# Optimization experiments

Measured on AMD Instinct MI355X. Metric: run time of the kernel, lower is better.

## Reference

```python
import jax, jax.numpy as jnp
import numpy as np


def setup_inputs() -> dict:
    key = jax.random.key(0)
    k1, k2, k3, k4, k5 = jax.random.split(key, 5)
    N, L, V = 8, 2048, 512
    E = 2 * V
    tokens = jax.random.randint(k1, (N, L, E), 0, 2, dtype=jnp.int64)
    s = 1.0 / np.sqrt(E)
    Wa_w = jax.random.uniform(k2, (E, E), jnp.float32, -s, s)
    Wa_b = jax.random.uniform(k3, (E,), jnp.float32, -s, s)
    Wb_w = jax.random.uniform(k4, (V, E), jnp.float32, -s, s)
    Wb_b = jax.random.uniform(k5, (V,), jnp.float32, -s, s)
    return {"tokens": tokens, "Wa_w": Wa_w, "Wa_b": Wa_b, "Wb_w": Wb_w, "Wb_b": Wb_b}


def reference(tokens, Wa_w, Wa_b, Wb_w, Wb_b):
    # x: [N, L, E] float embedding of binary tokens
    x = tokens.astype(jnp.float32)
    # q = Wa(x): [N, L, E] (torch Linear: x @ W^T + b)
    q = jnp.einsum("nle,fe->nlf", x, Wa_w) + Wa_b
    # scores: [N, L, L]; softmax over last dim
    scores = jnp.einsum("nlf,nmf->nlm", q, x)
    wts = jax.nn.softmax(scores, axis=-1)
    # a = wts @ x: [N, L, E]
    a = jnp.einsum("nlm,nme->nle", wts, x)
    # y = Wb(a): [N, L, V]; logits from last position
    y = jnp.einsum("nle,ve->nlv", a, Wb_w) + Wb_b
    logits = y[:, -1]  # [N, V]
    return logits
```

## Files before the change

### kernel.cpp

```cpp
#include <hip/hip_runtime.h>

#define NB 8
#define LS 2048
#define ED 1024
#define VD 512
#define CM 32
#define CH (LS / CM)
typedef unsigned long long u64;

__device__ inline float wave_reduce_sum(float v) {
    #pragma unroll
    for (int off = 32; off > 0; off >>= 1)
        v += __shfl_down(v, off, 64);
    return v;
}

__global__ void k_qrow(const int* __restrict__ tokens, const float* __restrict__ Wa_w,
                       const float* __restrict__ Wa_b, float* __restrict__ q_row) {
    int wid  = blockIdx.x * (blockDim.x >> 6) + (threadIdx.x >> 6);
    int lane = threadIdx.x & 63;
    int n = wid >> 10;
    int f = wid & (ED - 1);
    const int*   xrow = tokens + ((size_t)n * LS + (LS - 1)) * ED;
    const float* wrow = Wa_w + (size_t)f * ED;
    float acc = 0.f;
    #pragma unroll
    for (int k = 0; k < ED; k += 256) {
        int idx = k + lane * 4;
        int4   t = *reinterpret_cast<const int4*>(xrow + idx);
        float4 w = *reinterpret_cast<const float4*>(wrow + idx);
        acc += (float)t.x * w.x + (float)t.y * w.y + (float)t.z * w.z + (float)t.w * w.w;
    }
    acc = wave_reduce_sum(acc);
    if (lane == 0) q_row[wid] = acc + Wa_b[f];
}

__global__ __launch_bounds__(512) void k_flash(const int* __restrict__ tokens,
                                               const float* __restrict__ q_row,
                                               float* __restrict__ pa,
                                               float* __restrict__ mu_g,
                                               float* __restrict__ z_g) {
    int n = blockIdx.x >> 6;
    int c = blockIdx.x & (CH - 1);
    int t = threadIdx.x;
    int wave = t >> 6, lane = t & 63;

    __shared__ u64   pk[CM][16];
    __shared__ float s_lds[CM];
    __shared__ float p_lds[CM];

    const float* q = q_row + n * ED;

    #pragma unroll
    for (int i = 0; i < 4; ++i) {
        int m = wave + 8 * i;
        const int* row = tokens + ((size_t)(n * LS + c * CM + m)) * ED;
        float acc = 0.f;
        #pragma unroll
        for (int k = 0; k < ED; k += 256) {
            int idx = k + lane * 4;
            int4   tv = *reinterpret_cast<const int4*>(row + idx);
            float4 qv = *reinterpret_cast<const float4*>(q + idx);
            u64 b0 = __ballot(tv.x != 0);
            u64 b1 = __ballot(tv.y != 0);
            u64 b2 = __ballot(tv.z != 0);
            u64 b3 = __ballot(tv.w != 0);
            if (lane == 0) {
                int wb = (k >> 8) * 4;
                pk[m][wb + 0] = b0; pk[m][wb + 1] = b1;
                pk[m][wb + 2] = b2; pk[m][wb + 3] = b3;
            }
            acc += (float)tv.x * qv.x + (float)tv.y * qv.y
                 + (float)tv.z * qv.z + (float)tv.w * qv.w;
        }
        acc = wave_reduce_sum(acc);
        if (lane == 0) s_lds[m] = acc;
    }
    __syncthreads();

    if (wave == 0) {
        float s = (lane < CM) ? s_lds[lane] : -3.0e38f;
        float mx = s;
        #pragma unroll
        for (int off = 16; off > 0; off >>= 1) mx = fmaxf(mx, __shfl_xor(mx, off, 64));
        float p = (lane < CM) ? expf(s - mx) : 0.f;
        float z = p;
        #pragma unroll
        for (int off = 16; off > 0; off >>= 1) z += __shfl_xor(z, off, 64);
        if (lane < CM) p_lds[lane] = p;
        if (lane == 0) { mu_g[blockIdx.x] = mx; z_g[blockIdx.x] = z; }
    }
    __syncthreads();

    int w0  = ((t >> 8) << 2) | (t & 3);
    int bit = (t >> 2) & 63;
    float a0 = 0.f, a1 = 0.f;
    #pragma unroll 8
    for (int m = 0; m < CM; ++m) {
        float p  = p_lds[m];
        u64   lo = pk[m][w0];
        u64   hi = pk[m][w0 + 8];
        a0 += ((lo >> bit) & 1ull) ? p : 0.f;
        a1 += ((hi >> bit) & 1ull) ? p : 0.f;
    }
    float* par = pa + (size_t)blockIdx.x * ED;
    par[t]       = a0;
    par[t + 512] = a1;
}

__global__ __launch_bounds__(1024) void k_out(const float* __restrict__ pa,
                                              const float* __restrict__ mu_g,
                                              const float* __restrict__ z_g,
                                              const float* __restrict__ Wb_w,
                                              const float* __restrict__ Wb_b,
                                              float* __restrict__ out) {
    int n  = blockIdx.x >> 4;
    int vt = blockIdx.x & 15;
    int t  = threadIdx.x;
    int wave = t >> 6, lane = t & 63;
    __shared__ float coef[CH];
    __shared__ float a_lds[ED];

    if (wave == 0) {
        float m_c = mu_g[n * CH + lane];
        float mx = m_c;
        #pragma unroll
        for (int off = 32; off > 0; off >>= 1) mx = fmaxf(mx, __shfl_xor(mx, off, 64));
        float cf = expf(m_c - mx);
        float zc = z_g[n * CH + lane] * cf;
        float Z = zc;
        #pragma unroll
        for (int off = 32; off > 0; off >>= 1) Z += __shfl_xor(Z, off, 64);
        coef[lane] = cf / Z;
    }
    __syncthreads();

    float acc = 0.f;
    #pragma unroll
    for (int ci = 0; ci < CH; ++ci)
        acc += coef[ci] * pa[((size_t)(n * CH + ci)) * ED + t];
    a_lds[t] = acc;
    __syncthreads();

    #pragma unroll
    for (int i = 0; i < 2; ++i) {
        int v = vt * 32 + wave * 2 + i;
        const float* wr = Wb_w + (size_t)v * ED;
        float d = 0.f;
        #pragma unroll
        for (int k = 0; k < ED; k += 256) {
            int idx = k + lane * 4;
            float4 wv = *reinterpret_cast<const float4*>(wr + idx);
            float4 av = *reinterpret_cast<const float4*>(&a_lds[idx]);
            d += av.x * wv.x + av.y * wv.y + av.z * wv.z + av.w * wv.w;
        }
        d = wave_reduce_sum(d);
        if (lane == 0) out[n * VD + v] = d + Wb_b[v];
    }
}

extern "C" void kernel_launch(void* const* d_in, const int* in_sizes, int n_in,
                              void* d_out, int out_size, void* d_ws, size_t ws_size,
                              hipStream_t stream) {
    const int*   tokens = (const int*)  d_in[0];
    const float* Wa_w   = (const float*)d_in[1];
    const float* Wa_b   = (const float*)d_in[2];
    const float* Wb_w   = (const float*)d_in[3];
    const float* Wb_b   = (const float*)d_in[4];
    float* out = (float*)d_out;

    float* ws    = (float*)d_ws;
    float* q_row = ws;
    float* pa    = q_row + NB * ED;
    float* mu_g  = pa + (size_t)NB * CH * ED;
    float* z_g   = mu_g + NB * CH;

    k_qrow<<<dim3((NB * ED) / 4), dim3(256), 0, stream>>>(tokens, Wa_w, Wa_b, q_row);
    k_flash<<<dim3(NB * CH), dim3(512), 0, stream>>>(tokens, q_row, pa, mu_g, z_g);
    k_out<<<dim3(NB * 16), dim3(1024), 0, stream>>>(pa, mu_g, z_g, Wb_w, Wb_b, out);
}
```

Baseline: 31.61 us.

## Batch qrow over all batches per weight row, stage q in LDS, nontemporal token loads

```diff
diff --git a/kernel.cpp b/kernel.cpp
--- a/kernel.cpp
+++ b/kernel.cpp
@@ -7,6 +7,7 @@
 #define CM 32
 #define CH (LS / CM)
 typedef unsigned long long u64;
+typedef __attribute__((ext_vector_type(4))) int i32x4;
 
 __device__ inline float wave_reduce_sum(float v) {
     #pragma unroll
@@ -15,24 +16,41 @@
     return v;
 }
 
-__global__ void k_qrow(const int* __restrict__ tokens, const float* __restrict__ Wa_w,
-                       const float* __restrict__ Wa_b, float* __restrict__ q_row) {
-    int wid  = blockIdx.x * (blockDim.x >> 6) + (threadIdx.x >> 6);
-    int lane = threadIdx.x & 63;
-    int n = wid >> 10;
-    int f = wid & (ED - 1);
-    const int*   xrow = tokens + ((size_t)n * LS + (LS - 1)) * ED;
+__global__ __launch_bounds__(256) void k_qrow(const int* __restrict__ tokens,
+                                              const float* __restrict__ Wa_w,
+                                              const float* __restrict__ Wa_b,
+                                              float* __restrict__ q_row) {
+    __shared__ int xs[NB][ED];
+    int t = threadIdx.x;
+    #pragma unroll
+    for (int i = 0; i < 8; ++i) {
+        int v4 = i * 256 + t;
+        int n  = v4 >> 8;
+        int e  = (v4 & 255) * 4;
+        *reinterpret_cast<int4*>(&xs[n][e]) =
+            *reinterpret_cast<const int4*>(&tokens[((size_t)n * LS + (LS - 1)) * ED + e]);
+    }
+    __syncthreads();
+    int wave = t >> 6, lane = t & 63;
+    int f = blockIdx.x * 4 + wave;
     const float* wrow = Wa_w + (size_t)f * ED;
-    float acc = 0.f;
+    float acc[NB] = {0.f, 0.f, 0.f, 0.f, 0.f, 0.f, 0.f, 0.f};
     #pragma unroll
     for (int k = 0; k < ED; k += 256) {
         int idx = k + lane * 4;
-        int4   t = *reinterpret_cast<const int4*>(xrow + idx);
         float4 w = *reinterpret_cast<const float4*>(wrow + idx);
-        acc += (float)t.x * w.x + (float)t.y * w.y + (float)t.z * w.z + (float)t.w * w.w;
-    }
-    acc = wave_reduce_sum(acc);
-    if (lane == 0) q_row[wid] = acc + Wa_b[f];
+        #pragma unroll
+        for (int n = 0; n < NB; ++n) {
+            int4 tv = *reinterpret_cast<const int4*>(&xs[n][idx]);
+            acc[n] += (float)tv.x * w.x + (float)tv.y * w.y
+                    + (float)tv.z * w.z + (float)tv.w * w.w;
+        }
+    }
+    #pragma unroll
+    for (int n = 0; n < NB; ++n) {
+        float s = wave_reduce_sum(acc[n]);
+        if (lane == 0) q_row[n * ED + f] = s + Wa_b[f];
+    }
 }
 
 __global__ __launch_bounds__(512) void k_flash(const int* __restrict__ tokens,
@@ -46,10 +64,13 @@
     int wave = t >> 6, lane = t & 63;
 
     __shared__ u64   pk[CM][16];
+    __shared__ float q_lds[ED];
     __shared__ float s_lds[CM];
     __shared__ float p_lds[CM];
 
-    const float* q = q_row + n * ED;
+    *reinterpret_cast<float2*>(&q_lds[t * 2]) =
+        *reinterpret_cast<const float2*>(&q_row[n * ED + t * 2]);
+    __syncthreads();
 
     #pragma unroll
     for (int i = 0; i < 4; ++i) {
@@ -59,8 +80,8 @@
         #pragma unroll
         for (int k = 0; k < ED; k += 256) {
             int idx = k + lane * 4;
-            int4   tv = *reinterpret_cast<const int4*>(row + idx);
-            float4 qv = *reinterpret_cast<const float4*>(q + idx);
+            i32x4  tv = __builtin_nontemporal_load(reinterpret_cast<const i32x4*>(row + idx));
+            float4 qv = *reinterpret_cast<const float4*>(&q_lds[idx]);
             u64 b0 = __ballot(tv.x != 0);
             u64 b1 = __ballot(tv.y != 0);
             u64 b2 = __ballot(tv.z != 0);
@@ -175,7 +196,7 @@
     float* mu_g  = pa + (size_t)NB * CH * ED;
     float* z_g   = mu_g + NB * CH;
 
-    k_qrow<<<dim3((NB * ED) / 4), dim3(256), 0, stream>>>(tokens, Wa_w, Wa_b, q_row);
+    k_qrow<<<dim3(256), dim3(256), 0, stream>>>(tokens, Wa_w, Wa_b, q_row);
     k_flash<<<dim3(NB * CH), dim3(512), 0, stream>>>(tokens, q_row, pa, mu_g, z_g);
     k_out<<<dim3(NB * 16), dim3(1024), 0, stream>>>(pa, mu_g, z_g, Wb_w, Wb_b, out);
 }
```

New measurement: 36.13 us. 1.14x slower.

## Pack token bitmasks in a wide first kernel and score from packed bits

Applied to the files above, without the earlier changes.

```diff
diff --git a/kernel.cpp b/kernel.cpp
--- a/kernel.cpp
+++ b/kernel.cpp
@@ -15,28 +15,55 @@
     return v;
 }
 
-__global__ void k_qrow(const int* __restrict__ tokens, const float* __restrict__ Wa_w,
-                       const float* __restrict__ Wa_b, float* __restrict__ q_row) {
-    int wid  = blockIdx.x * (blockDim.x >> 6) + (threadIdx.x >> 6);
-    int lane = threadIdx.x & 63;
-    int n = wid >> 10;
-    int f = wid & (ED - 1);
-    const int*   xrow = tokens + ((size_t)n * LS + (LS - 1)) * ED;
-    const float* wrow = Wa_w + (size_t)f * ED;
-    float acc = 0.f;
-    #pragma unroll
-    for (int k = 0; k < ED; k += 256) {
-        int idx = k + lane * 4;
-        int4   t = *reinterpret_cast<const int4*>(xrow + idx);
-        float4 w = *reinterpret_cast<const float4*>(wrow + idx);
-        acc += (float)t.x * w.x + (float)t.y * w.y + (float)t.z * w.z + (float)t.w * w.w;
-    }
-    acc = wave_reduce_sum(acc);
-    if (lane == 0) q_row[wid] = acc + Wa_b[f];
-}
-
-__global__ __launch_bounds__(512) void k_flash(const int* __restrict__ tokens,
-                                               const float* __restrict__ q_row,
+__global__ __launch_bounds__(256) void k_pack_qrow(const int* __restrict__ tokens,
+                                                   const float* __restrict__ Wa_w,
+                                                   const float* __restrict__ Wa_b,
+                                                   float* __restrict__ q_row,
+                                                   u64* __restrict__ pk_g) {
+    int b = blockIdx.x, t = threadIdx.x;
+    int wave = t >> 6, lane = t & 63;
+    if (b < 1024) {
+        #pragma unroll
+        for (int i = 0; i < 4; ++i) {
+            int row = b * 16 + wave * 4 + i;
+            const int* xr = tokens + (size_t)row * ED;
+            u64* pkr = pk_g + (size_t)row * 16;
+            #pragma unroll
+            for (int k = 0; k < ED; k += 256) {
+                int idx = k + lane * 4;
+                int4 tv = *reinterpret_cast<const int4*>(xr + idx);
+                u64 b0 = __ballot(tv.x != 0);
+                u64 b1 = __ballot(tv.y != 0);
+                u64 b2 = __ballot(tv.z != 0);
+                u64 b3 = __ballot(tv.w != 0);
+                u64 bb = b0;
+                bb = (lane == 1) ? b1 : bb;
+                bb = (lane == 2) ? b2 : bb;
+                bb = (lane == 3) ? b3 : bb;
+                if (lane < 4) pkr[((k >> 8) << 2) + lane] = bb;
+            }
+        }
+    } else {
+        int wid = (b - 1024) * 4 + wave;
+        int n = wid >> 10, f = wid & (ED - 1);
+        const int*   xrow = tokens + ((size_t)n * LS + (LS - 1)) * ED;
+        const float* wrow = Wa_w + (size_t)f * ED;
+        float acc = 0.f;
+        #pragma unroll
+        for (int k = 0; k < ED; k += 256) {
+            int idx = k + lane * 4;
+            int4   tv = *reinterpret_cast<const int4*>(xrow + idx);
+            float4 w  = *reinterpret_cast<const float4*>(wrow + idx);
+            acc += (float)tv.x * w.x + (float)tv.y * w.y
+                 + (float)tv.z * w.z + (float)tv.w * w.w;
+        }
+        acc = wave_reduce_sum(acc);
+        if (lane == 0) q_row[wid] = acc + Wa_b[f];
+    }
+}
+
+__global__ __launch_bounds__(512) void k_flash(const float* __restrict__ q_row,
+                                               const u64* __restrict__ pk_g,
                                                float* __restrict__ pa,
                                                float* __restrict__ mu_g,
                                                float* __restrict__ z_g) {
@@ -45,33 +72,29 @@
     int t = threadIdx.x;
     int wave = t >> 6, lane = t & 63;
 
-    __shared__ u64   pk[CM][16];
+    __shared__ u64   pk[CM * 16];
+    __shared__ float q_perm[ED];
     __shared__ float s_lds[CM];
     __shared__ float p_lds[CM];
 
-    const float* q = q_row + n * ED;
+    pk[t] = pk_g[((size_t)(n * LS + c * CM)) * 16 + t];
+    {
+        float2 qq = *reinterpret_cast<const float2*>(&q_row[n * ED + t * 2]);
+        int e0 = t * 2, e1 = e0 + 1;
+        q_perm[((((e0 >> 8) << 2) | (e0 & 3)) << 6) | ((e0 >> 2) & 63)] = qq.x;
+        q_perm[((((e1 >> 8) << 2) | (e1 & 3)) << 6) | ((e1 >> 2) & 63)] = qq.y;
+    }
+    __syncthreads();
 
     #pragma unroll
     for (int i = 0; i < 4; ++i) {
         int m = wave + 8 * i;
-        const int* row = tokens + ((size_t)(n * LS + c * CM + m)) * ED;
         float acc = 0.f;
         #pragma unroll
-        for (int k = 0; k < ED; k += 256) {
-            int idx = k + lane * 4;
-            int4   tv = *reinterpret_cast<const int4*>(row + idx);
-            float4 qv = *reinterpret_cast<const float4*>(q + idx);
-            u64 b0 = __ballot(tv.x != 0);
-            u64 b1 = __ballot(tv.y != 0);
-            u64 b2 = __ballot(tv.z != 0);
-            u64 b3 = __ballot(tv.w != 0);
-            if (lane == 0) {
-                int wb = (k >> 8) * 4;
-                pk[m][wb + 0] = b0; pk[m][wb + 1] = b1;
-                pk[m][wb + 2] = b2; pk[m][wb + 3] = b3;
-            }
-            acc += (float)tv.x * qv.x + (float)tv.y * qv.y
-                 + (float)tv.z * qv.z + (float)tv.w * qv.w;
+        for (int w = 0; w < 16; ++w) {
+            u64   word = pk[m * 16 + w];
+            float qv   = q_perm[(w << 6) | lane];
+            acc += ((word >> lane) & 1ull) ? qv : 0.f;
         }
         acc = wave_reduce_sum(acc);
         if (lane == 0) s_lds[m] = acc;
@@ -98,8 +121,8 @@
     #pragma unroll 8
     for (int m = 0; m < CM; ++m) {
         float p  = p_lds[m];
-        u64   lo = pk[m][w0];
-        u64   hi = pk[m][w0 + 8];
+        u64   lo = pk[m * 16 + w0];
+        u64   hi = pk[m * 16 + w0 + 8];
         a0 += ((lo >> bit) & 1ull) ? p : 0.f;
         a1 += ((hi >> bit) & 1ull) ? p : 0.f;
     }
@@ -169,13 +192,13 @@
     const float* Wb_b   = (const float*)d_in[4];
     float* out = (float*)d_out;
 
-    float* ws    = (float*)d_ws;
-    float* q_row = ws;
+    u64*   pk_g  = (u64*)d_ws;
+    float* q_row = (float*)(pk_g + (size_t)NB * LS * 16);
     float* pa    = q_row + NB * ED;
     float* mu_g  = pa + (size_t)NB * CH * ED;
     float* z_g   = mu_g + NB * CH;
 
-    k_qrow<<<dim3((NB * ED) / 4), dim3(256), 0, stream>>>(tokens, Wa_w, Wa_b, q_row);
-    k_flash<<<dim3(NB * CH), dim3(512), 0, stream>>>(tokens, q_row, pa, mu_g, z_g);
+    k_pack_qrow<<<dim3(3072), dim3(256), 0, stream>>>(tokens, Wa_w, Wa_b, q_row, pk_g);
+    k_flash<<<dim3(NB * CH), dim3(512), 0, stream>>>(q_row, pk_g, pa, mu_g, z_g);
     k_out<<<dim3(NB * 16), dim3(1024), 0, stream>>>(pa, mu_g, z_g, Wb_w, Wb_b, out);
 }
```

New measurement: 32.92 us. 1.04x slower.
